# Kernel tuning notes

Hardware: AMD Instinct MI355X
Metric: run time of the kernel (lower is better)

The kernel has to match this reference:

```python
import jax, jax.numpy as jnp
import numpy as np

N, B, E = 10000, 4, 160000
C_IN, C_OUT, C_E = 64, 64, 16


def _mk_params(key, c_in, c_out, c_e):
    ks = jax.random.split(key, 8)
    s = 0.1
    return dict(
        w_n=jax.random.normal(ks[0], (c_in, c_out), jnp.float32) * s,
        w_e=jax.random.normal(ks[1], (c_e, c_out), jnp.float32) * s,
        q=jax.random.normal(ks[2], (c_out, c_out), jnp.float32) * s,
        k=jax.random.normal(ks[3], (c_out, c_out), jnp.float32) * s,
        aw=jax.random.normal(ks[4], (3 * c_out, 1), jnp.float32) * s,
        ab=jax.random.normal(ks[5], (1,), jnp.float32) * s,
        ow=jax.random.normal(ks[6], (2 * c_out, c_out), jnp.float32) * s,
        ob=jax.random.normal(ks[7], (c_out,), jnp.float32) * s,
    )


def setup_inputs() -> dict:
    key = jax.random.key(0)
    kx, ke, ka, k1, k2 = jax.random.split(key, 5)
    inp = {
        'X': jax.random.normal(kx, (N, B, C_IN), jnp.float32),
        'edge_index': jax.random.randint(ke, (2, E), 0, N, jnp.int32),
        'edge_attr': jax.random.normal(ka, (E, C_E), jnp.float32),
    }
    p1 = _mk_params(k1, C_IN, C_OUT, C_E)
    p2 = _mk_params(k2, C_OUT, C_OUT, C_E)
    for name, v in p1.items():
        inp[name + '1'] = v
    for name, v in p2.items():
        inp[name + '2'] = v
    return inp


def egnn_conv(x, edge_index, edge_attr, w_n, w_e, q, k, aw, ab, ow, ob, n_nodes):
    # x: [N,B,Cin]; edge_attr: [E,Ce]
    xp = x @ w_n                         # [N,B,C]
    ea = edge_attr @ w_e                 # [E,C]
    src, dst = edge_index[0], edge_index[1]
    xj = xp[src]                         # [E,B,C] gather (source)
    xi = xp[dst]                         # [E,B,C] gather (target)
    qf = xj @ q                          # [E,B,C]
    kf = xi @ k                          # [E,B,C]
    eab = jnp.broadcast_to(ea[:, None, :], qf.shape)  # [E,B,C]
    att_feat = jnp.concatenate([qf, kf, eab], axis=-1)  # [E,B,3C]
    att = jax.nn.sigmoid(att_feat @ aw + ab)            # [E,B,1]
    gate = jax.nn.sigmoid(eab)
    msg = att * xj * gate                # [E,B,C]
    aggr = jax.ops.segment_max(msg, dst, num_segments=n_nodes)  # [N,B,C]
    aggr = jnp.where(jnp.isneginf(aggr), 0.0, aggr)  # empty segments -> 0
    out = jnp.concatenate([xp, aggr], axis=-1) @ ow + ob
    return xp + out


def reference(X, edge_index, edge_attr,
              w_n1, w_e1, q1, k1, aw1, ab1, ow1, ob1,
              w_n2, w_e2, q2, k2, aw2, ab2, ow2, ob2):
    n_nodes = X.shape[0]
    c1 = egnn_conv(X, edge_index, edge_attr, w_n1, w_e1, q1, k1, aw1, ab1, ow1, ob1, n_nodes)
    c1 = jax.nn.leaky_relu(c1, 0.01)
    c2 = egnn_conv(c1, edge_index, edge_attr, w_n2, w_e2, q2, k2, aw2, ab2, ow2, ob2, n_nodes)
    c2 = jax.nn.leaky_relu(c2, 0.01)
    return c2
```

## Files before the change

kernel.cpp:

```cpp
#include <hip/hip_runtime.h>
#include <math.h>

#define NN 10000
#define BB 4
#define EE 160000
#define CC 64
#define CE 16

static constexpr size_t OFF_XPA    = 0;
static constexpr size_t OFF_XPB    = 10240000;
static constexpr size_t OFF_SA     = 20480000;
static constexpr size_t OFF_SB     = 20640000;
static constexpr size_t OFF_VECS   = 20800000;
static constexpr size_t OFF_COUNTS = 20801280;
static constexpr size_t OFF_CURSOR = 20841280;
static constexpr size_t OFF_OFFS   = 20881280;
static constexpr size_t OFF_RECS   = 20921344;
static constexpr size_t OFF_ATT    = 22201344;
static constexpr size_t OFF_SE2    = 24761344;
static constexpr size_t OFF_ORDER  = 25401344;


__device__ __forceinline__ float sigmoidf_(float x) {
    return __builtin_amdgcn_rcpf(1.0f + __expf(-x));
}

__device__ __forceinline__ float bcast_(float v, int l) {
    return __uint_as_float(__builtin_amdgcn_readlane(__float_as_uint(v), l));
}

__global__ void hist_vecs_kernel(const int* __restrict__ ei, int* __restrict__ counts,
                                 const float* __restrict__ q1, const float* __restrict__ k1,
                                 const float* __restrict__ aw1, const float* __restrict__ we1,
                                 const float* __restrict__ q2, const float* __restrict__ k2,
                                 const float* __restrict__ aw2, const float* __restrict__ we2,
                                 float* __restrict__ vecs) {
    int e = blockIdx.x * blockDim.x + threadIdx.x;
    if (e < EE) atomicAdd(&counts[ei[EE + e]], 1);
    if (blockIdx.x == 0) {
        int t = threadIdx.x;
        if (t < 64) {
            float a = 0.f, b = 0.f, c = 0.f, d = 0.f;
            for (int j = 0; j < 64; ++j) {
                a = fmaf(q1[t * 64 + j], aw1[j], a);
                b = fmaf(k1[t * 64 + j], aw1[64 + j], b);
                c = fmaf(q2[t * 64 + j], aw2[j], c);
                d = fmaf(k2[t * 64 + j], aw2[64 + j], d);
            }
            vecs[t] = a; vecs[64 + t] = b; vecs[144 + t] = c; vecs[208 + t] = d;
        }
        if (t < 16) {
            float a = 0.f, b = 0.f;
            for (int j = 0; j < 64; ++j) {
                a = fmaf(we1[t * 64 + j], aw1[128 + j], a);
                b = fmaf(we2[t * 64 + j], aw2[128 + j], b);
            }
            vecs[128 + t] = a; vecs[272 + t] = b;
        }
    }
}

__global__ __launch_bounds__(1024) void scan_order_kernel(const int* __restrict__ counts,
                                                          int* __restrict__ offs,
                                                          int* __restrict__ order) {
    __shared__ int hist[1024];
    __shared__ int cur[1024];
    __shared__ int startb[1024];
    __shared__ int wsum[16];
    int t = threadIdx.x;
    hist[t] = 0; cur[t] = 0;
    int lane = t & 63, wid = t >> 6;
    int v[10];
    int s = 0;
    #pragma unroll
    for (int j = 0; j < 10; ++j) {
        int i = t * 10 + j;
        v[j] = (i < NN) ? counts[i] : 0;
        s += v[j];
    }
    int ps = s;
    #pragma unroll
    for (int off = 1; off < 64; off <<= 1) {
        int u = __shfl_up(ps, off, 64);
        if (lane >= off) ps += u;
    }
    if (lane == 63) wsum[wid] = ps;
    __syncthreads();
    int wbase = 0;
    for (int w = 0; w < wid; ++w) wbase += wsum[w];
    int tb = wbase + ps - s;
    #pragma unroll
    for (int j = 0; j < 10; ++j) {
        int i = t * 10 + j;
        if (i < NN) offs[i] = tb;
        tb += v[j];
    }
    if (t == 1023) offs[NN] = tb;
    #pragma unroll
    for (int j = 0; j < 10; ++j) {
        int i = t * 10 + j;
        if (i < NN) {
            int d = v[j] > 1023 ? 1023 : v[j];
            atomicAdd(&hist[d], 1);
        }
    }
    __syncthreads();
    int r = 1023 - t;
    int hv = hist[r];
    int ps2 = hv;
    #pragma unroll
    for (int off = 1; off < 64; off <<= 1) {
        int u = __shfl_up(ps2, off, 64);
        if (lane >= off) ps2 += u;
    }
    if (lane == 63) wsum[wid] = ps2;
    __syncthreads();
    int wb2 = 0;
    for (int w = 0; w < wid; ++w) wb2 += wsum[w];
    startb[r] = wb2 + ps2 - hv;
    __syncthreads();
    #pragma unroll
    for (int j = 0; j < 10; ++j) {
        int i = t * 10 + j;
        if (i < NN) {
            int d = v[j] > 1023 ? 1023 : v[j];
            int pos = startb[d] + atomicAdd(&cur[d], 1);
            order[pos] = i;
        }
    }
}

__global__ __launch_bounds__(256) void node_prep_kernel(
    const float* __restrict__ x, const float* __restrict__ w_n,
    const float* __restrict__ qa, const float* __restrict__ ka,
    float* __restrict__ xp, float* __restrict__ sa, float* __restrict__ sb,
    int in_cm) {
    int t = threadIdx.x, wave = t >> 6, lane = t & 63;
    int node = blockIdx.x * 4 + wave;
    float4 xv = ((const float4*)(x + (size_t)node * BB * CC))[lane];
    float acc0 = 0.f, acc1 = 0.f, acc2 = 0.f, acc3 = 0.f;
    if (in_cm) {
        #pragma unroll
        for (int ci = 0; ci < 64; ++ci) {
            float w = w_n[ci * 64 + lane];
            acc0 = fmaf(bcast_(xv.x, ci), w, acc0);
            acc1 = fmaf(bcast_(xv.y, ci), w, acc1);
            acc2 = fmaf(bcast_(xv.z, ci), w, acc2);
            acc3 = fmaf(bcast_(xv.w, ci), w, acc3);
        }
    } else {
        #pragma unroll
        for (int ci = 0; ci < 64; ++ci) {
            float w = w_n[ci * 64 + lane];
            float c0 = ((ci & 3) == 0) ? xv.x : ((ci & 3) == 1) ? xv.y
                     : ((ci & 3) == 2) ? xv.z : xv.w;
            int src = ci >> 2;
            acc0 = fmaf(bcast_(c0, (0 << 4) | src), w, acc0);
            acc1 = fmaf(bcast_(c0, (1 << 4) | src), w, acc1);
            acc2 = fmaf(bcast_(c0, (2 << 4) | src), w, acc2);
            acc3 = fmaf(bcast_(c0, (3 << 4) | src), w, acc3);
        }
    }
    ((float4*)(xp + (size_t)node * BB * CC))[lane] =
        make_float4(acc0, acc1, acc2, acc3);
    float qv = qa[lane], kv = ka[lane];
    float ra0 = acc0 * qv, ra1 = acc1 * qv, ra2 = acc2 * qv, ra3 = acc3 * qv;
    float rb0 = acc0 * kv, rb1 = acc1 * kv, rb2 = acc2 * kv, rb3 = acc3 * kv;
    #pragma unroll
    for (int off = 32; off >= 1; off >>= 1) {
        ra0 += __shfl_xor(ra0, off, 64); ra1 += __shfl_xor(ra1, off, 64);
        ra2 += __shfl_xor(ra2, off, 64); ra3 += __shfl_xor(ra3, off, 64);
        rb0 += __shfl_xor(rb0, off, 64); rb1 += __shfl_xor(rb1, off, 64);
        rb2 += __shfl_xor(rb2, off, 64); rb3 += __shfl_xor(rb3, off, 64);
    }
    if (lane == 0) {
        sa[node * BB + 0] = ra0; sa[node * BB + 1] = ra1;
        sa[node * BB + 2] = ra2; sa[node * BB + 3] = ra3;
        sb[node * BB + 0] = rb0; sb[node * BB + 1] = rb1;
        sb[node * BB + 2] = rb2; sb[node * BB + 3] = rb3;
    }
}

__global__ __launch_bounds__(256) void scatter_kernel(
    const int* __restrict__ ei, const int* __restrict__ offs,
    int* __restrict__ cursor, const float* __restrict__ attr,
    const float* __restrict__ vecs, const float* __restrict__ ab1,
    const float* __restrict__ ab2, const float* __restrict__ sa,
    const float* __restrict__ sb, int2* __restrict__ recs,
    float* __restrict__ se2, float4* __restrict__ att) {
    int e = blockIdx.x * blockDim.x + threadIdx.x;
    if (e >= EE) return;
    int s = ei[e], d = ei[EE + e];
    const float4* ap = (const float4*)(attr + (size_t)e * CE);
    float4 a0 = ap[0], a1 = ap[1], a2 = ap[2], a3 = ap[3];
    const float* v1 = vecs + 128;
    const float* v2 = vecs + 272;
    float s1 = ab1[0], s2 = ab2[0];
    s1 = fmaf(a0.x, v1[0], s1);  s1 = fmaf(a0.y, v1[1], s1);
    s1 = fmaf(a0.z, v1[2], s1);  s1 = fmaf(a0.w, v1[3], s1);
    s1 = fmaf(a1.x, v1[4], s1);  s1 = fmaf(a1.y, v1[5], s1);
    s1 = fmaf(a1.z, v1[6], s1);  s1 = fmaf(a1.w, v1[7], s1);
    s1 = fmaf(a2.x, v1[8], s1);  s1 = fmaf(a2.y, v1[9], s1);
    s1 = fmaf(a2.z, v1[10], s1); s1 = fmaf(a2.w, v1[11], s1);
    s1 = fmaf(a3.x, v1[12], s1); s1 = fmaf(a3.y, v1[13], s1);
    s1 = fmaf(a3.z, v1[14], s1); s1 = fmaf(a3.w, v1[15], s1);
    s2 = fmaf(a0.x, v2[0], s2);  s2 = fmaf(a0.y, v2[1], s2);
    s2 = fmaf(a0.z, v2[2], s2);  s2 = fmaf(a0.w, v2[3], s2);
    s2 = fmaf(a1.x, v2[4], s2);  s2 = fmaf(a1.y, v2[5], s2);
    s2 = fmaf(a1.z, v2[6], s2);  s2 = fmaf(a1.w, v2[7], s2);
    s2 = fmaf(a2.x, v2[8], s2);  s2 = fmaf(a2.y, v2[9], s2);
    s2 = fmaf(a2.z, v2[10], s2); s2 = fmaf(a2.w, v2[11], s2);
    s2 = fmaf(a3.x, v2[12], s2); s2 = fmaf(a3.y, v2[13], s2);
    s2 = fmaf(a3.z, v2[14], s2); s2 = fmaf(a3.w, v2[15], s2);
    int p = atomicAdd(&cursor[d], 1);
    recs[offs[d] + p] = make_int2(s, e);
    se2[e] = s2;
    float4 sas = *(const float4*)(sa + (size_t)s * BB);
    float4 sbn = *(const float4*)(sb + (size_t)d * BB);
    float4 r;
    r.x = sigmoidf_(sas.x + sbn.x + s1);
    r.y = sigmoidf_(sas.y + sbn.y + s1);
    r.z = sigmoidf_(sas.z + sbn.z + s1);
    r.w = sigmoidf_(sas.w + sbn.w + s1);
    att[e] = r;
}

__global__ __launch_bounds__(256) void att_kernel(
    const int* __restrict__ ei, const float* __restrict__ se2,
    const float* __restrict__ sa, const float* __restrict__ sb,
    float4* __restrict__ att) {
    int e = blockIdx.x * blockDim.x + threadIdx.x;
    if (e >= EE) return;
    int s = ei[e], d = ei[EE + e];
    float se = se2[e];
    float4 sas = *(const float4*)(sa + (size_t)s * BB);
    float4 sbn = *(const float4*)(sb + (size_t)d * BB);
    float4 r;
    r.x = sigmoidf_(sas.x + sbn.x + se);
    r.y = sigmoidf_(sas.y + sbn.y + se);
    r.z = sigmoidf_(sas.z + sbn.z + se);
    r.w = sigmoidf_(sas.w + sbn.w + se);
    att[e] = r;
}

__global__ __launch_bounds__(256) void conv_out_kernel(
    const float* __restrict__ xp,
    const int2* __restrict__ recs,
    const int* __restrict__ offs,
    const float* __restrict__ attr,
    const float* __restrict__ w_e,
    const float4* __restrict__ att,
    const float* __restrict__ ow,
    const float* __restrict__ ob,
    const int* __restrict__ order,
    float* __restrict__ out,
    int out_std) {
    int t = threadIdx.x;
    int wave = t >> 6, lane = t & 63;
    int node = order[blockIdx.x * 4 + wave];

    float wec[CE];
    #pragma unroll
    for (int j = 0; j < CE; ++j) wec[j] = w_e[j * CC + lane];

    float4 xnv = ((const float4*)(xp + (size_t)node * BB * CC))[lane];
    float xn0 = xnv.x, xn1 = xnv.y, xn2 = xnv.z, xn3 = xnv.w;

    int o0 = offs[node], o1 = offs[node + 1];
    float m0 = -INFINITY, m1 = -INFINITY, m2 = -INFINITY, m3 = -INFINITY;

    int i = o0;
    int2 rec = (i < o1) ? recs[i] : make_int2(0, 0);
    while (i < o1) {
        int2 cur = rec;
        ++i;
        if (i < o1) rec = recs[i];
        int s = cur.x, e = cur.y;
        float4 at = att[e];
        const float4* ap = (const float4*)(attr + (size_t)e * CE);
        float4 a0 = ap[0], a1 = ap[1], a2 = ap[2], a3 = ap[3];
        float g = 0.f;
        g = fmaf(a0.x, wec[0], g);  g = fmaf(a0.y, wec[1], g);
        g = fmaf(a0.z, wec[2], g);  g = fmaf(a0.w, wec[3], g);
        g = fmaf(a1.x, wec[4], g);  g = fmaf(a1.y, wec[5], g);
        g = fmaf(a1.z, wec[6], g);  g = fmaf(a1.w, wec[7], g);
        g = fmaf(a2.x, wec[8], g);  g = fmaf(a2.y, wec[9], g);
        g = fmaf(a2.z, wec[10], g); g = fmaf(a2.w, wec[11], g);
        g = fmaf(a3.x, wec[12], g); g = fmaf(a3.y, wec[13], g);
        g = fmaf(a3.z, wec[14], g); g = fmaf(a3.w, wec[15], g);
        g = sigmoidf_(g);
        float4 xv4 = ((const float4*)(xp + (size_t)s * BB * CC))[lane];
        m0 = fmaxf(m0, at.x * xv4.x * g);
        m1 = fmaxf(m1, at.y * xv4.y * g);
        m2 = fmaxf(m2, at.z * xv4.z * g);
        m3 = fmaxf(m3, at.w * xv4.w * g);
    }
    m0 = (m0 == -INFINITY) ? 0.f : m0;
    m1 = (m1 == -INFINITY) ? 0.f : m1;
    m2 = (m2 == -INFINITY) ? 0.f : m2;
    m3 = (m3 == -INFINITY) ? 0.f : m3;

    float o0f = 0.f, o1f = 0.f, o2f = 0.f, o3f = 0.f;
    #pragma unroll
    for (int ci = 0; ci < 64; ++ci) {
        float wa = ow[ci * 64 + lane];
        float wb = ow[(64 + ci) * 64 + lane];
        o0f = fmaf(bcast_(xn0, ci), wa, o0f);
        o1f = fmaf(bcast_(xn1, ci), wa, o1f);
        o2f = fmaf(bcast_(xn2, ci), wa, o2f);
        o3f = fmaf(bcast_(xn3, ci), wa, o3f);
        o0f = fmaf(bcast_(m0, ci), wb, o0f);
        o1f = fmaf(bcast_(m1, ci), wb, o1f);
        o2f = fmaf(bcast_(m2, ci), wb, o2f);
        o3f = fmaf(bcast_(m3, ci), wb, o3f);
    }
    float obv = ob[lane];
    float r0 = xn0 + o0f + obv;
    float r1 = xn1 + o1f + obv;
    float r2 = xn2 + o2f + obv;
    float r3 = xn3 + o3f + obv;
    r0 = (r0 > 0.f) ? r0 : 0.01f * r0;
    r1 = (r1 > 0.f) ? r1 : 0.01f * r1;
    r2 = (r2 > 0.f) ? r2 : 0.01f * r2;
    r3 = (r3 > 0.f) ? r3 : 0.01f * r3;
    if (out_std) {
        float* op = out + (size_t)node * BB * CC + lane;
        op[0] = r0; op[64] = r1; op[128] = r2; op[192] = r3;
    } else {
        ((float4*)(out + (size_t)node * BB * CC))[lane] =
            make_float4(r0, r1, r2, r3);
    }
}

extern "C" void kernel_launch(void* const* d_in, const int* in_sizes, int n_in,
                              void* d_out, int out_size, void* d_ws, size_t ws_size,
                              hipStream_t stream) {
    const float* X    = (const float*)d_in[0];
    const int*   ei   = (const int*)d_in[1];
    const float* attr = (const float*)d_in[2];
    const float* w_n1 = (const float*)d_in[3];
    const float* w_e1 = (const float*)d_in[4];
    const float* q1   = (const float*)d_in[5];
    const float* k1   = (const float*)d_in[6];
    const float* aw1  = (const float*)d_in[7];
    const float* ab1  = (const float*)d_in[8];
    const float* ow1  = (const float*)d_in[9];
    const float* ob1  = (const float*)d_in[10];
    const float* w_n2 = (const float*)d_in[11];
    const float* w_e2 = (const float*)d_in[12];
    const float* q2   = (const float*)d_in[13];
    const float* k2   = (const float*)d_in[14];
    const float* aw2  = (const float*)d_in[15];
    const float* ab2  = (const float*)d_in[16];
    const float* ow2  = (const float*)d_in[17];
    const float* ob2  = (const float*)d_in[18];
    float* out = (float*)d_out;

    char* ws = (char*)d_ws;
    float*  xpA    = (float*)(ws + OFF_XPA);
    float*  xpB    = (float*)(ws + OFF_XPB);
    float*  sa     = (float*)(ws + OFF_SA);
    float*  sb     = (float*)(ws + OFF_SB);
    float*  vecs   = (float*)(ws + OFF_VECS);
    int*    counts = (int*)(ws + OFF_COUNTS);
    int*    cursor = (int*)(ws + OFF_CURSOR);
    int*    offs   = (int*)(ws + OFF_OFFS);
    int2*   recs   = (int2*)(ws + OFF_RECS);
    float4* att    = (float4*)(ws + OFF_ATT);
    float*  se2    = (float*)(ws + OFF_SE2);
    int*    order  = (int*)(ws + OFF_ORDER);

    hipMemsetAsync(counts, 0, 2 * NN * sizeof(int), stream);
    hist_vecs_kernel<<<EE / 256, 256, 0, stream>>>(ei, counts, q1, k1, aw1, w_e1,
                                                   q2, k2, aw2, w_e2, vecs);
    node_prep_kernel<<<NN / 4, 256, 0, stream>>>(X, w_n1, vecs + 0, vecs + 64,
                                                 xpA, sa, sb, 0);
    scan_order_kernel<<<1, 1024, 0, stream>>>(counts, offs, order);
    scatter_kernel<<<EE / 256, 256, 0, stream>>>(ei, offs, cursor, attr, vecs,
                                                 ab1, ab2, sa, sb, recs, se2, att);
    conv_out_kernel<<<NN / 4, 256, 0, stream>>>(xpA, recs, offs, attr, w_e1, att,
                                                ow1, ob1, order, xpB, 0);
    node_prep_kernel<<<NN / 4, 256, 0, stream>>>(xpB, w_n2, vecs + 144, vecs + 208,
                                                 xpA, sa, sb, 1);
    att_kernel<<<EE / 256, 256, 0, stream>>>(ei, se2, sa, sb, att);
    conv_out_kernel<<<NN / 4, 256, 0, stream>>>(xpA, recs, offs, attr, w_e2, att,
                                                ow2, ob2, order, out, 1);
}
```

Measured before the change: 270.9 us.

## Split each node's edge loop across two waves and merge maxima via LDS

conv_out_kernel now assigns two waves per destination node instead of one. Each wave scans half of the node's incoming edges, and the partial maxima are combined through shared memory. Each wave then computes the output projection for two of the four batch slices, halving per-wave FMA work in the epilogue. The goal is to shorten the serial per-node gather loop and double parallelism. The cost is a block-wide barrier, LDS traffic, redundant loads of w_e and xp per wave, and twice as many blocks.

```diff
diff --git a/kernel.cpp b/kernel.cpp
--- a/kernel.cpp
+++ b/kernel.cpp
@@ -255,26 +255,31 @@
     const int* __restrict__ order,
     float* __restrict__ out,
     int out_std) {
+    __shared__ float part[4][BB * CC];
     int t = threadIdx.x;
     int wave = t >> 6, lane = t & 63;
-    int node = order[blockIdx.x * 4 + wave];
+    int half = wave & 1;
+    int node = order[blockIdx.x * 2 + (wave >> 1)];
 
     float wec[CE];
     #pragma unroll
     for (int j = 0; j < CE; ++j) wec[j] = w_e[j * CC + lane];
 
     float4 xnv = ((const float4*)(xp + (size_t)node * BB * CC))[lane];
-    float xn0 = xnv.x, xn1 = xnv.y, xn2 = xnv.z, xn3 = xnv.w;
 
     int o0 = offs[node], o1 = offs[node + 1];
+    int n = o1 - o0;
+    int nh = (n + 1) >> 1;
+    int ib = o0 + half * nh;
+    int ie = half ? o1 : (o0 + nh);
+
     float m0 = -INFINITY, m1 = -INFINITY, m2 = -INFINITY, m3 = -INFINITY;
-
-    int i = o0;
-    int2 rec = (i < o1) ? recs[i] : make_int2(0, 0);
-    while (i < o1) {
+    int i = ib;
+    int2 rec = (i < ie) ? recs[i] : make_int2(0, 0);
+    while (i < ie) {
         int2 cur = rec;
         ++i;
-        if (i < o1) rec = recs[i];
+        if (i < ie) rec = recs[i];
         int s = cur.x, e = cur.y;
         float4 at = att[e];
         const float4* ap = (const float4*)(attr + (size_t)e * CE);
@@ -295,40 +300,44 @@
         m2 = fmaxf(m2, at.z * xv4.z * g);
         m3 = fmaxf(m3, at.w * xv4.w * g);
     }
-    m0 = (m0 == -INFINITY) ? 0.f : m0;
-    m1 = (m1 == -INFINITY) ? 0.f : m1;
-    m2 = (m2 == -INFINITY) ? 0.f : m2;
-    m3 = (m3 == -INFINITY) ? 0.f : m3;
-
-    float o0f = 0.f, o1f = 0.f, o2f = 0.f, o3f = 0.f;
+
+    part[wave][0 * CC + lane] = m0;
+    part[wave][1 * CC + lane] = m1;
+    part[wave][2 * CC + lane] = m2;
+    part[wave][3 * CC + lane] = m3;
+    __syncthreads();
+    int pw = wave ^ 1;
+    int b0 = half * 2, b1 = half * 2 + 1;
+    float mo0 = half ? m2 : m0;
+    float mo1 = half ? m3 : m1;
+    float mm0 = fmaxf(mo0, part[pw][b0 * CC + lane]);
+    float mm1 = fmaxf(mo1, part[pw][b1 * CC + lane]);
+    mm0 = (mm0 == -INFINITY) ? 0.f : mm0;
+    mm1 = (mm1 == -INFINITY) ? 0.f : mm1;
+    float xn0 = half ? xnv.z : xnv.x;
+    float xn1 = half ? xnv.w : xnv.y;
+
+    float o0f = 0.f, o1f = 0.f;
     #pragma unroll
     for (int ci = 0; ci < 64; ++ci) {
         float wa = ow[ci * 64 + lane];
         float wb = ow[(64 + ci) * 64 + lane];
         o0f = fmaf(bcast_(xn0, ci), wa, o0f);
         o1f = fmaf(bcast_(xn1, ci), wa, o1f);
-        o2f = fmaf(bcast_(xn2, ci), wa, o2f);
-        o3f = fmaf(bcast_(xn3, ci), wa, o3f);
-        o0f = fmaf(bcast_(m0, ci), wb, o0f);
-        o1f = fmaf(bcast_(m1, ci), wb, o1f);
-        o2f = fmaf(bcast_(m2, ci), wb, o2f);
-        o3f = fmaf(bcast_(m3, ci), wb, o3f);
+        o0f = fmaf(bcast_(mm0, ci), wb, o0f);
+        o1f = fmaf(bcast_(mm1, ci), wb, o1f);
     }
     float obv = ob[lane];
     float r0 = xn0 + o0f + obv;
     float r1 = xn1 + o1f + obv;
-    float r2 = xn2 + o2f + obv;
-    float r3 = xn3 + o3f + obv;
     r0 = (r0 > 0.f) ? r0 : 0.01f * r0;
     r1 = (r1 > 0.f) ? r1 : 0.01f * r1;
-    r2 = (r2 > 0.f) ? r2 : 0.01f * r2;
-    r3 = (r3 > 0.f) ? r3 : 0.01f * r3;
     if (out_std) {
         float* op = out + (size_t)node * BB * CC + lane;
-        op[0] = r0; op[64] = r1; op[128] = r2; op[192] = r3;
+        op[b0 * CC] = r0; op[b1 * CC] = r1;
     } else {
-        ((float4*)(out + (size_t)node * BB * CC))[lane] =
-            make_float4(r0, r1, r2, r3);
+        *(float2*)(out + (size_t)node * BB * CC + lane * 4 + b0) =
+            make_float2(r0, r1);
     }
 }
 
@@ -378,11 +387,11 @@
     scan_order_kernel<<<1, 1024, 0, stream>>>(counts, offs, order);
     scatter_kernel<<<EE / 256, 256, 0, stream>>>(ei, offs, cursor, attr, vecs,
                                                  ab1, ab2, sa, sb, recs, se2, att);
-    conv_out_kernel<<<NN / 4, 256, 0, stream>>>(xpA, recs, offs, attr, w_e1, att,
+    conv_out_kernel<<<NN / 2, 256, 0, stream>>>(xpA, recs, offs, attr, w_e1, att,
                                                 ow1, ob1, order, xpB, 0);
     node_prep_kernel<<<NN / 4, 256, 0, stream>>>(xpB, w_n2, vecs + 144, vecs + 208,
                                                  xpA, sa, sb, 1);
     att_kernel<<<EE / 256, 256, 0, stream>>>(ei, se2, sa, sb, att);
-    conv_out_kernel<<<NN / 4, 256, 0, stream>>>(xpA, recs, offs, attr, w_e2, att,
+    conv_out_kernel<<<NN / 2, 256, 0, stream>>>(xpA, recs, offs, attr, w_e2, att,
                                                 ow2, ob2, order, out, 1);
 }
```

Result: slower. 284.7 us (+5.1%).
